# Optimization experiments

Measured on AMD Instinct MI355X. Metric: run time of the kernel, lower is better.

The kernel has to match this reference:

```python
import jax, jax.numpy as jnp
import numpy as np

# ---- polar grid config (matches init_kwargs) ----
N_RADIAL = 48
N_ANGULAR = 72
RADIAL_EDGES = jnp.arange(2.0, 51.0, dtype=jnp.float32)            # 49 edges, [2, 50] m
ANGLE_EDGES = jnp.linspace(-np.pi, np.pi, N_ANGULAR + 1).astype(jnp.float32)
Z_MIN, Z_MAX = -3.0, 5.0
MAX_PTS = 64      # max_points_per_voxel
MAX_VOX = 3000    # max_voxels (< H = 3456, truncation path active)
H = N_RADIAL * N_ANGULAR


def setup_inputs() -> dict:
    key = jax.random.key(0)
    pts = jax.random.normal(key, (4_000_000, 5), dtype=jnp.float32)
    # scale xy to ~[-45,45] m and z to ~[-6,6] m so masks keep a realistic fraction
    scale = jnp.array([15.0, 15.0, 2.0, 1.0, 1.0], dtype=jnp.float32)
    return {"points": pts * scale}


def reference(points):
    N, C = points.shape
    x, y, z = points[:, 0], points[:, 1], points[:, 2]
    r = jnp.sqrt(x * x + y * y)
    theta = jnp.arctan2(y, x)

    valid = ((z >= Z_MIN) & (z < Z_MAX)
             & (r >= RADIAL_EDGES[0]) & (r < RADIAL_EDGES[-1])
             & (theta >= ANGLE_EDGES[0]) & (theta < ANGLE_EDGES[-1]))

    # torch.searchsorted(right=False) == jnp side='left'
    r_idx = jnp.clip(jnp.searchsorted(RADIAL_EDGES, r, side='left') - 1, 0, N_RADIAL - 1)
    t_idx = jnp.clip(jnp.searchsorted(ANGLE_EDGES, theta, side='left') - 1, 0, N_ANGULAR - 1)

    # invalid points get sentinel hash H (out of range -> dropped by scatter)
    vhash = jnp.where(valid, r_idx * N_ANGULAR + t_idx, H).astype(jnp.int32)

    # sort points by voxel hash (stable, matching torch.argsort semantics here)
    order = jnp.argsort(vhash)
    sh = vhash[order]                       # [N] sorted hashes
    sp = points[order]                      # [N, C] points in hash order

    # rank of each point within its voxel = position - first occurrence of its hash
    first = jnp.searchsorted(sh, sh, side='left')
    rank = jnp.arange(N, dtype=jnp.int32) - first.astype(jnp.int32)

    # dense hard-voxelization scatter: keep first MAX_PTS points per voxel.
    # out-of-range (sh==H or rank>=MAX_PTS) indices are dropped.
    vox_dense = jnp.zeros((H, MAX_PTS, C), dtype=points.dtype).at[sh, rank].set(sp, mode='drop')

    counts = jax.ops.segment_sum(jnp.ones_like(vhash), vhash, num_segments=H + 1)[:H]
    npts_dense = jnp.minimum(counts, MAX_PTS).astype(jnp.int32)

    # unique occupied hashes in ascending order -> output slots (first MAX_VOX kept)
    occupied = counts > 0
    slot = jnp.cumsum(occupied.astype(jnp.int32)) - 1
    slot = jnp.where(occupied & (slot < MAX_VOX), slot, MAX_VOX)  # MAX_VOX => dropped
    slot2hash = jnp.zeros((MAX_VOX,), jnp.int32).at[slot].set(jnp.arange(H, dtype=jnp.int32), mode='drop')
    slot_valid = jnp.zeros((MAX_VOX,), bool).at[slot].set(True, mode='drop')

    voxels = jnp.where(slot_valid[:, None, None], vox_dense[slot2hash], 0.0)  # [MAX_VOX, MAX_PTS, C]
    num_points = jnp.where(slot_valid, npts_dense[slot2hash], 0)

    ri = slot2hash // N_ANGULAR
    ti = slot2hash % N_ANGULAR
    coords = jnp.where(slot_valid[:, None],
                       jnp.stack([ri, ti, jnp.zeros_like(ri)], axis=1), 0).astype(jnp.int32)

    r_c = 0.5 * (RADIAL_EDGES[ri] + RADIAL_EDGES[ri + 1])
    t_c = 0.5 * (ANGLE_EDGES[ti] + ANGLE_EDGES[ti + 1])
    centers = jnp.where(slot_valid[:, None],
                        jnp.stack([r_c * jnp.cos(t_c), r_c * jnp.sin(t_c)], axis=1), 0.0)

    return voxels, coords, num_points, centers
```

## Files before the change

kernel.cpp:

```cpp
#include <hip/hip_runtime.h>
#include <math.h>

#define NRAD 48
#define NANG 72
#define HV   3456
#define HVW  864
#define MAXP 64
#define MAXV 3000
#define BLK  256
#define CHT  64
#define TILE 4096
#define SUBT 1024
#define NCH  16

#define OFF_C   (MAXV*MAXP*5)
#define OFF_N   (OFF_C + MAXV*3)
#define OFF_X   (OFF_N + MAXV)

#define PI_F 3.14159265358979323846f

__device__ __forceinline__ float angle_edge(int j) {
  const double PI = 3.14159265358979311599796346854;
  const double step = (PI - (-PI)) / 72.0;
  if (j == 72) return (float)PI;
  return (float)(-PI + (double)j * step);
}

__device__ __forceinline__ int point_bin(float x, float y, float z,
                                         const float* __restrict__ eang,
                                         const float* __restrict__ ec,
                                         const float* __restrict__ es) {
  float r = __fsqrt_rn(__fadd_rn(__fmul_rn(x, x), __fmul_rn(y, y)));
  if (!(z >= -3.0f && z < 5.0f && r >= 2.0f && r < 50.0f)) return HV;
  int ri = (int)ceilf(r) - 3;
  ri = max(0, min(NRAD - 1, ri));
  float ax = fabsf(x), ay = fabsf(y);
  float u = fminf(ax, ay), U = fmaxf(ax, ay);
  bool big = u > 0.41421356f * U;
  float num = big ? (U - u) : u;
  float den = big ? (U + u) : U;
  float v = num * __builtin_amdgcn_rcpf(den);
  float s2 = v * v;
  float pp = v * (1.0f + s2 * (-0.33333333f + s2 * (0.2f - s2 * 0.14285714f)));
  float th1 = big ? (0.78539816f - pp) : pp;
  if (ay > ax) th1 = 1.57079633f - th1;
  if (x < 0.0f) th1 = PI_F - th1;
  float that = copysignf(th1, y);
  int g = (int)floorf((that + PI_F) * 11.459155902616465f);
  g = max(0, min(NANG - 1, g));
  float GA = 2e-6f * r;
  bool unc = false;
  for (;;) {
    float d = __fmaf_rn(ec[g], y, -__fmul_rn(es[g], x));
    if (d > GA) break;
    if (d > -GA || g == 0) { unc = true; break; }
    --g;
  }
  if (!unc) {
    while (g < NANG - 1) {
      float d = __fmaf_rn(ec[g + 1], y, -__fmul_rn(es[g + 1], x));
      if (d < -GA) break;
      if (d <= GA) { unc = true; break; }
      ++g;
    }
    if (!unc && g == NANG - 1) {
      float d = __fmaf_rn(ec[72], y, -__fmul_rn(es[72], x));
      if (d >= -GA) unc = true;
    }
  }
  if (!unc) return ri * NANG + g;
  float th = (float)atan2((double)y, (double)x);
  if (!(th >= eang[0] && th < eang[72])) return HV;
  int gg = g;
  while (gg > 0 && !(eang[gg] < th)) gg--;
  while (gg < NANG - 1 && eang[gg + 1] < th) gg++;
  return ri * NANG + max(0, min(NANG - 1, gg));
}

__global__ __launch_bounds__(BLK) void k_hist(
    const float* __restrict__ pts, int N, int tile, int n4, int tailN,
    unsigned char* __restrict__ hist, unsigned short* __restrict__ bins,
    float4* __restrict__ out4) {
  __shared__ int lh[HV];
  __shared__ float eang[73], ec[73], es[73];
  int t = blockIdx.x, tid = threadIdx.x;
  for (int j = t * BLK + tid; j < n4; j += gridDim.x * BLK)
    out4[j] = make_float4(0.f, 0.f, 0.f, 0.f);
  if (t == 0 && tid < tailN) ((float*)out4)[(size_t)n4 * 4 + tid] = 0.f;
  for (int i = tid; i < HV; i += BLK) lh[i] = 0;
  if (tid < 73) {
    float e = angle_edge(tid);
    eang[tid] = e;
    ec[tid] = (float)cos((double)e);
    es[tid] = (float)sin((double)e);
  }
  __syncthreads();
  int base = t * tile;
  int end  = min(base + tile, N);
  int endq = base + (((end - base) >> 2) << 2);
  const float4* p4 = (const float4*)pts;
  for (int i0 = base + (tid << 2); i0 < endq; i0 += (BLK << 2)) {
    size_t q = (size_t)(i0 >> 2) * 5;
    float4 v0 = p4[q], v1 = p4[q + 1], v2 = p4[q + 2], v3 = p4[q + 3], v4 = p4[q + 4];
    int b0 = point_bin(v0.x, v0.y, v0.z, eang, ec, es);
    int b1 = point_bin(v1.y, v1.z, v1.w, eang, ec, es);
    int b2 = point_bin(v2.z, v2.w, v3.x, eang, ec, es);
    int b3 = point_bin(v3.w, v4.x, v4.y, eang, ec, es);
    *(ushort4*)(bins + i0) = make_ushort4((unsigned short)b0, (unsigned short)b1,
                                          (unsigned short)b2, (unsigned short)b3);
    if (b0 < HV) atomicAdd(&lh[b0], 1);
    if (b1 < HV) atomicAdd(&lh[b1], 1);
    if (b2 < HV) atomicAdd(&lh[b2], 1);
    if (b3 < HV) atomicAdd(&lh[b3], 1);
  }
  for (int i = endq + tid; i < end; i += BLK) {
    size_t p = (size_t)i * 5;
    int b = point_bin(pts[p], pts[p + 1], pts[p + 2], eang, ec, es);
    bins[i] = (unsigned short)b;
    if (b < HV) atomicAdd(&lh[b], 1);
  }
  __syncthreads();
  unsigned char* ht = hist + (size_t)t * HV;
  for (int i = tid; i < HV; i += BLK) ht[i] = (unsigned char)min(lh[i], 64);
}

__global__ void k_scan_a(const unsigned int* __restrict__ hist32, int NT,
                         unsigned int* __restrict__ part32) {
  int w = blockIdx.x * BLK + threadIdx.x;
  int c = blockIdx.y;
  if (w >= HVW) return;
  int t0 = c * CHT, t1 = min(t0 + CHT, NT);
  int s0 = 0, s1 = 0, s2 = 0, s3 = 0;
  for (int t = t0; t < t1; ++t) {
    unsigned int v = hist32[(size_t)t * HVW + w];
    s0 = min(s0 + (int)(v & 255u), 64);
    s1 = min(s1 + (int)((v >> 8) & 255u), 64);
    s2 = min(s2 + (int)((v >> 16) & 255u), 64);
    s3 = min(s3 + (int)(v >> 24), 64);
  }
  part32[(size_t)c * HVW + w] = (unsigned)s0 | ((unsigned)s1 << 8) |
                                ((unsigned)s2 << 16) | ((unsigned)s3 << 24);
}

__global__ __launch_bounds__(1024) void k_bsc(unsigned int* __restrict__ part32, int NC,
                                              int* __restrict__ soh,
                                              float* __restrict__ out) {
  __shared__ float eang[73];
  __shared__ int ssum[1024];
  int tid = threadIdx.x;
  if (tid < 73) eang[tid] = angle_edge(tid);
  int r0 = 0, r1 = 0, r2 = 0, r3 = 0;
  for (int cb = 0; cb < NC; cb += 16) {
    unsigned int vv[16];
#pragma unroll
    for (int k = 0; k < 16; ++k) {
      int c = cb + k;
      vv[k] = (tid < HVW && c < NC) ? part32[(size_t)c * HVW + tid] : 0u;
    }
#pragma unroll
    for (int k = 0; k < 16; ++k) {
      int c = cb + k;
      if (tid < HVW && c < NC)
        part32[(size_t)c * HVW + tid] = (unsigned)r0 | ((unsigned)r1 << 8) |
                                        ((unsigned)r2 << 16) | ((unsigned)r3 << 24);
      r0 = min(r0 + (int)(vv[k] & 255u), 64);
      r1 = min(r1 + (int)((vv[k] >> 8) & 255u), 64);
      r2 = min(r2 + (int)((vv[k] >> 16) & 255u), 64);
      r3 = min(r3 + (int)(vv[k] >> 24), 64);
    }
  }
  int c0 = r0, c1 = r1, c2 = r2, c3 = r3;
  int occ = (c0 > 0) + (c1 > 0) + (c2 > 0) + (c3 > 0);
  if (tid >= HVW) occ = 0;
  ssum[tid] = occ;
  __syncthreads();
  for (int off = 1; off < 1024; off <<= 1) {
    int v = (tid >= off) ? ssum[tid - off] : 0;
    __syncthreads();
    ssum[tid] += v;
    __syncthreads();
  }
  int base = ssum[tid] - occ;
  if (tid < HVW) {
    int cs[4] = {c0, c1, c2, c3};
#pragma unroll
    for (int k = 0; k < 4; ++k) {
      int h = tid * 4 + k;
      int cnt = cs[k];
      int s = -1;
      if (cnt > 0) {
        if (base < MAXV) s = base;
        base++;
      }
      soh[h] = s;
      if (s >= 0) {
        int ri = h / NANG, ti = h % NANG;
        out[OFF_C + s * 3 + 0] = (float)ri;
        out[OFF_C + s * 3 + 1] = (float)ti;
        out[OFF_C + s * 3 + 2] = 0.0f;
        out[OFF_N + s] = (float)cnt;
        float rc = 2.5f + (float)ri;
        float tc = 0.5f * (eang[ti] + eang[ti + 1]);
        out[OFF_X + s * 2 + 0] = rc * cosf(tc);
        out[OFF_X + s * 2 + 1] = rc * sinf(tc);
      }
    }
  }
}

__global__ void k_scan_c(unsigned int* __restrict__ hist32, int NT,
                         const unsigned int* __restrict__ part32) {
  int w = blockIdx.x * BLK + threadIdx.x;
  int c = blockIdx.y;
  if (w >= HVW) return;
  int t0 = c * CHT, t1 = min(t0 + CHT, NT);
  unsigned int pv = part32[(size_t)c * HVW + w];
  int r0 = pv & 255u, r1 = (pv >> 8) & 255u, r2 = (pv >> 16) & 255u, r3 = pv >> 24;
  for (int t = t0; t < t1; ++t) {
    size_t o = (size_t)t * HVW + w;
    unsigned int v = hist32[o];
    hist32[o] = (unsigned)r0 | ((unsigned)r1 << 8) |
                ((unsigned)r2 << 16) | ((unsigned)r3 << 24);
    r0 = min(r0 + (int)(v & 255u), 64);
    r1 = min(r1 + (int)((v >> 8) & 255u), 64);
    r2 = min(r2 + (int)((v >> 16) & 255u), 64);
    r3 = min(r3 + (int)(v >> 24), 64);
  }
}

__global__ __launch_bounds__(BLK) void k_scatter_fast(
    const float* __restrict__ pts, int N,
    const unsigned char* __restrict__ hist, const unsigned short* __restrict__ bins,
    const int* __restrict__ soh, float* __restrict__ out) {
  __shared__ unsigned int whd[4 * HV / 2];
  unsigned short (*wh)[HV] = (unsigned short (*)[HV])whd;
  int t = blockIdx.x;
  int tid = threadIdx.x;
  int lane = tid & 63, wv = tid >> 6;
  for (int i = tid; i < 4 * HV / 2; i += BLK) whd[i] = 0u;
  __syncthreads();
  int base = t * TILE;
  int end  = min(base + TILE, N);
  int sb = base + wv * SUBT;
  int se = min(sb + SUBT, end);
  const unsigned char* ht = hist + (size_t)t * HV;
  unsigned short lb[NCH], lr[NCH];
  const unsigned long long lmask = (1ULL << lane) - 1ULL;
#pragma unroll
  for (int c = 0; c < NCH; ++c) {
    int i = sb + c * 64 + lane;
    int b = 4095;
    if (i < se) {
      int bi = bins[i];
      if (bi < HV && ht[bi] < 64) b = bi;
    }
    lb[c] = (unsigned short)b;
    lr[c] = 0;
    if (__ballot(b != 4095) == 0ULL) continue;
    unsigned long long m = ~0ULL;
#pragma unroll
    for (int k = 0; k < 12; ++k) {
      unsigned long long bal = __ballot((b >> k) & 1);
      m &= ((b >> k) & 1) ? bal : ~bal;
    }
    int rho = __popcll(m & lmask);
    int kap = __popcll(m);
    int cv = 0;
    if (b != 4095) {
      cv = wh[wv][b];
      if (rho == 0) wh[wv][b] = (unsigned short)(cv + kap);
    }
    lr[c] = (unsigned short)(cv + rho);
  }
  __syncthreads();
  for (int j = tid; j < HV; j += BLK) {
    int a0 = wh[0][j], a1 = wh[1][j], a2 = wh[2][j];
    wh[0][j] = 0;
    wh[1][j] = (unsigned short)a0;
    wh[2][j] = (unsigned short)(a0 + a1);
    wh[3][j] = (unsigned short)(a0 + a1 + a2);
  }
  __syncthreads();
#pragma unroll
  for (int c = 0; c < NCH; ++c) {
    int b = lb[c];
    if (b == 4095) continue;
    int rank = (int)ht[b] + (int)wh[wv][b] + (int)lr[c];
    if (rank < MAXP) {
      int s = soh[b];
      if (s >= 0) {
        int i = sb + c * 64 + lane;
        size_t dst = (size_t)(s * MAXP + rank) * 5;
        size_t src = (size_t)i * 5;
        out[dst + 0] = pts[src + 0];
        out[dst + 1] = pts[src + 1];
        out[dst + 2] = pts[src + 2];
        out[dst + 3] = pts[src + 3];
        out[dst + 4] = pts[src + 4];
      }
    }
  }
}

__global__ void k_scatter_gen(const float* __restrict__ pts, int N, int tile,
                              const unsigned char* __restrict__ hist,
                              const unsigned short* __restrict__ bins,
                              const int* __restrict__ soh,
                              float* __restrict__ out) {
  __shared__ int cur[HV + 1];
  int t = blockIdx.x;
  int tid = threadIdx.x;
  const unsigned char* ht = hist + (size_t)t * HV;
  for (int i = tid; i < HV + 1; i += BLK) cur[i] = (i < HV) ? (int)ht[i] : 0;
  __syncthreads();
  int base = t * tile;
  int end  = min(base + tile, N);
  int lane = tid & 63, wv = tid >> 6;
  for (int g = base; g < base + tile; g += BLK) {
    int i = g + tid;
    bool act = (i < end);
    int b = act ? (int)bins[i] : 0x10000;
    int rho = 0, kap = 0;
    for (int j = 0; j < 64; ++j) {
      int bj = __shfl(b, j, 64);
      if (bj == b) { kap++; if (j < lane) rho++; }
    }
    int rank = 0x7FFFFFFF;
    for (int w = 0; w < 4; ++w) {
      if (wv == w && act) {
        int bs = cur[b];
        rank = bs + rho;
        if (rho == 0) cur[b] = bs + kap;
      }
      __syncthreads();
    }
    if (act && rank < MAXP && b < HV) {
      int s = soh[b];
      if (s >= 0) {
        size_t dst = (size_t)(s * MAXP + rank) * 5;
        size_t src = (size_t)i * 5;
        out[dst + 0] = pts[src + 0];
        out[dst + 1] = pts[src + 1];
        out[dst + 2] = pts[src + 2];
        out[dst + 3] = pts[src + 3];
        out[dst + 4] = pts[src + 4];
      }
    }
  }
}

extern "C" void kernel_launch(void* const* d_in, const int* in_sizes, int n_in,
                              void* d_out, int out_size, void* d_ws, size_t ws_size,
                              hipStream_t stream) {
  const float* pts = (const float*)d_in[0];
  int N = in_sizes[0] / 5;
  float* out = (float*)d_out;

  auto align = [](size_t x) { return (x + 255) & ~(size_t)255; };
  int tile = TILE, NT = 1, NC = 1;
  size_t o_hist = 0, o_part = 0, o_soh = 0, o_bins = 0;
  for (;;) {
    NT = (N + tile - 1) / tile;
    NC = (NT + CHT - 1) / CHT;
    o_hist = 0;
    o_part = align(o_hist + (size_t)NT * HV);
    o_soh  = align(o_part + (size_t)NC * HV);
    o_bins = align(o_soh + (size_t)HV * 4);
    size_t need = o_bins + (size_t)N * 2;
    if (need <= ws_size || tile >= (1 << 22)) break;
    tile <<= 1;
  }

  char* w = (char*)d_ws;
  unsigned char* hist = (unsigned char*)(w + o_hist);
  unsigned int*  hist32 = (unsigned int*)hist;
  unsigned int*  part32 = (unsigned int*)(w + o_part);
  int* soh = (int*)(w + o_soh);
  unsigned short* bins = (unsigned short*)(w + o_bins);

  int n4 = out_size / 4;
  int tailN = out_size - n4 * 4;

  k_hist<<<NT, BLK, 0, stream>>>(pts, N, tile, n4, tailN, hist, bins, (float4*)out);
  dim3 ga((HVW + BLK - 1) / BLK, NC);
  k_scan_a<<<ga, BLK, 0, stream>>>(hist32, NT, part32);
  k_bsc<<<1, 1024, 0, stream>>>(part32, NC, soh, out);
  k_scan_c<<<ga, BLK, 0, stream>>>(hist32, NT, part32);
  if (tile == TILE) {
    k_scatter_fast<<<NT, BLK, 0, stream>>>(pts, N, hist, bins, soh, out);
  } else {
    k_scatter_gen<<<NT, BLK, 0, stream>>>(pts, N, tile, hist, bins, soh, out);
  }
}
```

Baseline: 93.47 us.

## Merge block scan and carry-propagate kernels, replace atan2 fallback with double edge tests

Merges the single-block global prefix kernel and the carry-apply kernel into one launch. In it, each chunk block recomputes its own carry by summing the earlier chunk partials, and one extra block builds the slot table. This removes a serial single-block pass and one kernel launch, and the chunk size is reduced to 16 tiles so more blocks run in parallel. The uncertain-angle fallback now uses double-precision cross products against precomputed midpoint boundaries instead of a double atan2 plus a search. That removes the costly atan2, but exact agreement with the reference binning depends on the boundary construction.

Result: faster. 88.28 us (median of 2 runs) (-5.6%).

```diff
diff --git a/kernel.cpp b/kernel.cpp
--- a/kernel.cpp
+++ b/kernel.cpp
@@ -8,7 +8,7 @@
 #define MAXP 64
 #define MAXV 3000
 #define BLK  256
-#define CHT  64
+#define CHT  16
 #define TILE 4096
 #define SUBT 1024
 #define NCH  16
@@ -26,10 +26,24 @@
   return (float)(-PI + (double)j * step);
 }
 
+__device__ __forceinline__ float next_up_f(float e) {
+  if (e == 0.0f) return __uint_as_float(1u);
+  unsigned u = __float_as_uint(e);
+  u = (e > 0.0f) ? (u + 1u) : (u - 1u);
+  return __uint_as_float(u);
+}
+__device__ __forceinline__ float next_dn_f(float e) {
+  if (e == 0.0f) return -__uint_as_float(1u);
+  unsigned u = __float_as_uint(e);
+  u = (e > 0.0f) ? (u - 1u) : (u + 1u);
+  return __uint_as_float(u);
+}
+
 __device__ __forceinline__ int point_bin(float x, float y, float z,
-                                         const float* __restrict__ eang,
                                          const float* __restrict__ ec,
-                                         const float* __restrict__ es) {
+                                         const float* __restrict__ es,
+                                         const double* __restrict__ cB,
+                                         const double* __restrict__ sB) {
   float r = __fsqrt_rn(__fadd_rn(__fmul_rn(x, x), __fmul_rn(y, y)));
   if (!(z >= -3.0f && z < 5.0f && r >= 2.0f && r < 50.0f)) return HV;
   int ri = (int)ceilf(r) - 3;
@@ -65,16 +79,28 @@
     }
     if (!unc && g == NANG - 1) {
       float d = __fmaf_rn(ec[72], y, -__fmul_rn(es[72], x));
-      if (d >= -GA) unc = true;
-    }
-  }
-  if (!unc) return ri * NANG + g;
-  float th = (float)atan2((double)y, (double)x);
-  if (!(th >= eang[0] && th < eang[72])) return HV;
-  int gg = g;
-  while (gg > 0 && !(eang[gg] < th)) gg--;
-  while (gg < NANG - 1 && eang[gg + 1] < th) gg++;
-  return ri * NANG + max(0, min(NANG - 1, gg));
+      if (d >= -GA) unc = true; else return ri * NANG + g;
+    } else if (!unc) {
+      return ri * NANG + g;
+    }
+  }
+  double xd = (double)x, yd = (double)y;
+  for (;;) {
+    if (g == 0) break;
+    double d = cB[g] * yd - sB[g] * xd;
+    if (d > 0.0) break;
+    --g;
+  }
+  while (g < NANG - 1) {
+    double d = cB[g + 1] * yd - sB[g + 1] * xd;
+    if (!(d > 0.0)) break;
+    ++g;
+  }
+  if (g == NANG - 1) {
+    double d = cB[72] * yd - sB[72] * xd;
+    if (d >= 0.0) return HV;
+  }
+  return ri * NANG + g;
 }
 
 __global__ __launch_bounds__(BLK) void k_hist(
@@ -82,7 +108,8 @@
     unsigned char* __restrict__ hist, unsigned short* __restrict__ bins,
     float4* __restrict__ out4) {
   __shared__ int lh[HV];
-  __shared__ float eang[73], ec[73], es[73];
+  __shared__ float ec[73], es[73];
+  __shared__ double cB[73], sB[73];
   int t = blockIdx.x, tid = threadIdx.x;
   for (int j = t * BLK + tid; j < n4; j += gridDim.x * BLK)
     out4[j] = make_float4(0.f, 0.f, 0.f, 0.f);
@@ -90,9 +117,14 @@
   for (int i = tid; i < HV; i += BLK) lh[i] = 0;
   if (tid < 73) {
     float e = angle_edge(tid);
-    eang[tid] = e;
-    ec[tid] = (float)cos((double)e);
-    es[tid] = (float)sin((double)e);
+    double ed = (double)e;
+    ec[tid] = (float)cos(ed);
+    es[tid] = (float)sin(ed);
+    double bnd;
+    if (tid < 72) bnd = ed + 0.5 * ((double)next_up_f(e) - ed);
+    else          bnd = ed - 0.5 * (ed - (double)next_dn_f(e));
+    cB[tid] = cos(bnd);
+    sB[tid] = sin(bnd);
   }
   __syncthreads();
   int base = t * tile;
@@ -102,10 +134,10 @@
   for (int i0 = base + (tid << 2); i0 < endq; i0 += (BLK << 2)) {
     size_t q = (size_t)(i0 >> 2) * 5;
     float4 v0 = p4[q], v1 = p4[q + 1], v2 = p4[q + 2], v3 = p4[q + 3], v4 = p4[q + 4];
-    int b0 = point_bin(v0.x, v0.y, v0.z, eang, ec, es);
-    int b1 = point_bin(v1.y, v1.z, v1.w, eang, ec, es);
-    int b2 = point_bin(v2.z, v2.w, v3.x, eang, ec, es);
-    int b3 = point_bin(v3.w, v4.x, v4.y, eang, ec, es);
+    int b0 = point_bin(v0.x, v0.y, v0.z, ec, es, cB, sB);
+    int b1 = point_bin(v1.y, v1.z, v1.w, ec, es, cB, sB);
+    int b2 = point_bin(v2.z, v2.w, v3.x, ec, es, cB, sB);
+    int b3 = point_bin(v3.w, v4.x, v4.y, ec, es, cB, sB);
     *(ushort4*)(bins + i0) = make_ushort4((unsigned short)b0, (unsigned short)b1,
                                           (unsigned short)b2, (unsigned short)b3);
     if (b0 < HV) atomicAdd(&lh[b0], 1);
@@ -115,7 +147,7 @@
   }
   for (int i = endq + tid; i < end; i += BLK) {
     size_t p = (size_t)i * 5;
-    int b = point_bin(pts[p], pts[p + 1], pts[p + 2], eang, ec, es);
+    int b = point_bin(pts[p], pts[p + 1], pts[p + 2], ec, es, cB, sB);
     bins[i] = (unsigned short)b;
     if (b < HV) atomicAdd(&lh[b], 1);
   }
@@ -142,89 +174,82 @@
                                 ((unsigned)s2 << 16) | ((unsigned)s3 << 24);
 }
 
-__global__ __launch_bounds__(1024) void k_bsc(unsigned int* __restrict__ part32, int NC,
-                                              int* __restrict__ soh,
-                                              float* __restrict__ out) {
-  __shared__ float eang[73];
-  __shared__ int ssum[1024];
+__global__ __launch_bounds__(1024) void k_scan_cb(
+    unsigned int* __restrict__ hist32, int NT, int NC,
+    const unsigned int* __restrict__ part32,
+    int* __restrict__ soh, float* __restrict__ out) {
+  int blk = blockIdx.x;
   int tid = threadIdx.x;
-  if (tid < 73) eang[tid] = angle_edge(tid);
-  int r0 = 0, r1 = 0, r2 = 0, r3 = 0;
-  for (int cb = 0; cb < NC; cb += 16) {
-    unsigned int vv[16];
+  if (blk < NC) {
+    if (tid >= HVW) return;
+    int r0 = 0, r1 = 0, r2 = 0, r3 = 0;
+    for (int cc = 0; cc < blk; ++cc) {
+      unsigned int v = part32[(size_t)cc * HVW + tid];
+      r0 = min(r0 + (int)(v & 255u), 64);
+      r1 = min(r1 + (int)((v >> 8) & 255u), 64);
+      r2 = min(r2 + (int)((v >> 16) & 255u), 64);
+      r3 = min(r3 + (int)(v >> 24), 64);
+    }
+    int t0 = blk * CHT, t1 = min(t0 + CHT, NT);
+    for (int t = t0; t < t1; ++t) {
+      size_t o = (size_t)t * HVW + tid;
+      unsigned int v = hist32[o];
+      hist32[o] = (unsigned)r0 | ((unsigned)r1 << 8) |
+                  ((unsigned)r2 << 16) | ((unsigned)r3 << 24);
+      r0 = min(r0 + (int)(v & 255u), 64);
+      r1 = min(r1 + (int)((v >> 8) & 255u), 64);
+      r2 = min(r2 + (int)((v >> 16) & 255u), 64);
+      r3 = min(r3 + (int)(v >> 24), 64);
+    }
+  } else {
+    __shared__ float eang[73];
+    __shared__ int ssum[1024];
+    if (tid < 73) eang[tid] = angle_edge(tid);
+    int c0 = 0, c1 = 0, c2 = 0, c3 = 0;
+    if (tid < HVW) {
+      for (int cc = 0; cc < NC; ++cc) {
+        unsigned int v = part32[(size_t)cc * HVW + tid];
+        c0 = min(c0 + (int)(v & 255u), 64);
+        c1 = min(c1 + (int)((v >> 8) & 255u), 64);
+        c2 = min(c2 + (int)((v >> 16) & 255u), 64);
+        c3 = min(c3 + (int)(v >> 24), 64);
+      }
+    }
+    int occ = (c0 > 0) + (c1 > 0) + (c2 > 0) + (c3 > 0);
+    ssum[tid] = occ;
+    __syncthreads();
+    for (int off = 1; off < 1024; off <<= 1) {
+      int v = (tid >= off) ? ssum[tid - off] : 0;
+      __syncthreads();
+      ssum[tid] += v;
+      __syncthreads();
+    }
+    int base = ssum[tid] - occ;
+    if (tid < HVW) {
+      int cs[4] = {c0, c1, c2, c3};
 #pragma unroll
-    for (int k = 0; k < 16; ++k) {
-      int c = cb + k;
-      vv[k] = (tid < HVW && c < NC) ? part32[(size_t)c * HVW + tid] : 0u;
-    }
-#pragma unroll
-    for (int k = 0; k < 16; ++k) {
-      int c = cb + k;
-      if (tid < HVW && c < NC)
-        part32[(size_t)c * HVW + tid] = (unsigned)r0 | ((unsigned)r1 << 8) |
-                                        ((unsigned)r2 << 16) | ((unsigned)r3 << 24);
-      r0 = min(r0 + (int)(vv[k] & 255u), 64);
-      r1 = min(r1 + (int)((vv[k] >> 8) & 255u), 64);
-      r2 = min(r2 + (int)((vv[k] >> 16) & 255u), 64);
-      r3 = min(r3 + (int)(vv[k] >> 24), 64);
-    }
-  }
-  int c0 = r0, c1 = r1, c2 = r2, c3 = r3;
-  int occ = (c0 > 0) + (c1 > 0) + (c2 > 0) + (c3 > 0);
-  if (tid >= HVW) occ = 0;
-  ssum[tid] = occ;
-  __syncthreads();
-  for (int off = 1; off < 1024; off <<= 1) {
-    int v = (tid >= off) ? ssum[tid - off] : 0;
-    __syncthreads();
-    ssum[tid] += v;
-    __syncthreads();
-  }
-  int base = ssum[tid] - occ;
-  if (tid < HVW) {
-    int cs[4] = {c0, c1, c2, c3};
-#pragma unroll
-    for (int k = 0; k < 4; ++k) {
-      int h = tid * 4 + k;
-      int cnt = cs[k];
-      int s = -1;
-      if (cnt > 0) {
-        if (base < MAXV) s = base;
-        base++;
+      for (int k = 0; k < 4; ++k) {
+        int h = tid * 4 + k;
+        int cnt = cs[k];
+        int s = -1;
+        if (cnt > 0) {
+          if (base < MAXV) s = base;
+          base++;
+        }
+        soh[h] = s;
+        if (s >= 0) {
+          int ri = h / NANG, ti = h % NANG;
+          out[OFF_C + s * 3 + 0] = (float)ri;
+          out[OFF_C + s * 3 + 1] = (float)ti;
+          out[OFF_C + s * 3 + 2] = 0.0f;
+          out[OFF_N + s] = (float)cnt;
+          float rc = 2.5f + (float)ri;
+          float tc = 0.5f * (eang[ti] + eang[ti + 1]);
+          out[OFF_X + s * 2 + 0] = rc * cosf(tc);
+          out[OFF_X + s * 2 + 1] = rc * sinf(tc);
+        }
       }
-      soh[h] = s;
-      if (s >= 0) {
-        int ri = h / NANG, ti = h % NANG;
-        out[OFF_C + s * 3 + 0] = (float)ri;
-        out[OFF_C + s * 3 + 1] = (float)ti;
-        out[OFF_C + s * 3 + 2] = 0.0f;
-        out[OFF_N + s] = (float)cnt;
-        float rc = 2.5f + (float)ri;
-        float tc = 0.5f * (eang[ti] + eang[ti + 1]);
-        out[OFF_X + s * 2 + 0] = rc * cosf(tc);
-        out[OFF_X + s * 2 + 1] = rc * sinf(tc);
-      }
-    }
-  }
-}
-
-__global__ void k_scan_c(unsigned int* __restrict__ hist32, int NT,
-                         const unsigned int* __restrict__ part32) {
-  int w = blockIdx.x * BLK + threadIdx.x;
-  int c = blockIdx.y;
-  if (w >= HVW) return;
-  int t0 = c * CHT, t1 = min(t0 + CHT, NT);
-  unsigned int pv = part32[(size_t)c * HVW + w];
-  int r0 = pv & 255u, r1 = (pv >> 8) & 255u, r2 = (pv >> 16) & 255u, r3 = pv >> 24;
-  for (int t = t0; t < t1; ++t) {
-    size_t o = (size_t)t * HVW + w;
-    unsigned int v = hist32[o];
-    hist32[o] = (unsigned)r0 | ((unsigned)r1 << 8) |
-                ((unsigned)r2 << 16) | ((unsigned)r3 << 24);
-    r0 = min(r0 + (int)(v & 255u), 64);
-    r1 = min(r1 + (int)((v >> 8) & 255u), 64);
-    r2 = min(r2 + (int)((v >> 16) & 255u), 64);
-    r3 = min(r3 + (int)(v >> 24), 64);
+    }
   }
 }
 
@@ -384,8 +409,7 @@
   k_hist<<<NT, BLK, 0, stream>>>(pts, N, tile, n4, tailN, hist, bins, (float4*)out);
   dim3 ga((HVW + BLK - 1) / BLK, NC);
   k_scan_a<<<ga, BLK, 0, stream>>>(hist32, NT, part32);
-  k_bsc<<<1, 1024, 0, stream>>>(part32, NC, soh, out);
-  k_scan_c<<<ga, BLK, 0, stream>>>(hist32, NT, part32);
+  k_scan_cb<<<NC + 1, 1024, 0, stream>>>(hist32, NT, NC, part32, soh, out);
   if (tile == TILE) {
     k_scatter_fast<<<NT, BLK, 0, stream>>>(pts, N, hist, bins, soh, out);
   } else {
```
